# Kernel optimization log

Hardware: AMD Instinct MI355X
Metric: run time of the kernel (lower is better)

Reference implementation:

```python
import jax, jax.numpy as jnp
import numpy as np
from math import factorial

L_MAX = 8
N_POINTS = 1_000_000


def _make_F(l_max):
    n = (l_max + 1) * (l_max + 2) // 2
    F = np.empty((n,), dtype=np.float64)
    for l in range(l_max + 1):
        for m in range(l + 1):
            F[l * (l + 1) // 2 + m] = (-1) ** m * np.sqrt(
                (2 * l + 1) / (2 * np.pi) * factorial(l - m) / factorial(l + m)
            )
    return jnp.asarray(F, dtype=jnp.float32)


def setup_inputs() -> dict:
    key = jax.random.key(0)
    xyz = jax.random.normal(key, (N_POINTS, 3), dtype=jnp.float32)
    F = _make_F(L_MAX)
    return {"xyz": xyz, "F": F}


def reference(xyz, F):
    l_max = L_MAX
    # normalize to unit sphere
    rsq = jnp.sum(xyz ** 2, axis=1)
    u = xyz / jnp.sqrt(rsq)[:, None]
    x, y, z = u[:, 0], u[:, 1], u[:, 2]

    # associated-Legendre-like recurrence (same math/signs as the torch module)
    Q = {(0, 0): jnp.ones_like(x)}
    for l in range(1, l_max + 1):
        Q[(l, l)] = -(2 * l - 1) * Q[(l - 1, l - 1)]
        Q[(l, l - 1)] = -z * Q[(l, l)]
        for m in range(0, l - 1):
            Q[(l, m)] = ((2 * l - 1) * z * Q[(l - 1, m)] - (l + m - 1) * Q[(l - 2, m)]) / (l - m)

    # trig recurrence: s_m = Im[(x+iy)^m], c_m = Re[(x+iy)^m]
    s = [jnp.zeros_like(x)]
    c = [jnp.ones_like(x)]
    for m in range(1, l_max + 1):
        s.append(x * s[m - 1] + y * c[m - 1])
        c.append(x * c[m - 1] - y * s[m - 1])

    inv_sqrt2 = 1.0 / np.sqrt(2.0)
    cols = []  # ordered as Y[:, l*l + l + m]
    for l in range(l_max + 1):
        base = l * (l + 1) // 2
        for m in range(-l, 0):
            cols.append(F[base - m] * Q[(l, -m)] * s[-m])
        cols.append(F[base] * Q[(l, 0)] * inv_sqrt2)
        for m in range(1, l + 1):
            cols.append(F[base + m] * Q[(l, m)] * c[m])
    return jnp.stack(cols, axis=1)  # [N, (l_max+1)^2]
```

## Files before the change

### kernel.cpp

```cpp
#include <hip/hip_runtime.h>

constexpr int LMAX = 8;
constexpr int NCOL = (LMAX + 1) * (LMAX + 1);
constexpr int PTS  = 64;
constexpr int TILE_FLOATS = PTS * NCOL;
constexpr int VEC4_ITERS  = TILE_FLOATS / 4 / PTS;

__device__ __forceinline__ void emit_col(float* row, const float* __restrict__ F,
                                         int l, int m, float Q, float sm, float cm) {
    const int fbase = l * (l + 1) / 2;
    const int cbase = l * l + l;
    if (m == 0) {
        const float inv_sqrt2 = 0.70710678118654752440f;
        row[cbase] = F[fbase] * Q * inv_sqrt2;
    } else {
        float t = F[fbase + m] * Q;
        row[cbase - m] = t * sm;
        row[cbase + m] = t * cm;
    }
}

__global__ __launch_bounds__(PTS) void sh_kernel(const float* __restrict__ xyz,
                                                 const float* __restrict__ F,
                                                 float* __restrict__ out, int n) {
    __shared__ float tile[TILE_FLOATS];
    const int lane    = threadIdx.x;
    const int base_pt = blockIdx.x * PTS;
    const int i       = base_pt + lane;

    float x = 0.0f, y = 0.0f, z = 1.0f;
    if (i < n) {
        x = xyz[3 * i + 0];
        y = xyz[3 * i + 1];
        z = xyz[3 * i + 2];
    }
    const float rsq  = x * x + y * y + z * z;
    const float rinv = rsqrtf(rsq);
    x *= rinv; y *= rinv; z *= rinv;

    float* row = &tile[lane * NCOL];

    float Qmm = 1.0f;
    float sm = 0.0f, cm = 1.0f;

#pragma unroll
    for (int m = 0; m <= LMAX; ++m) {
        if (m > 0) {
            Qmm = -(float)(2 * m - 1) * Qmm;
            const float s_new = x * sm + y * cm;
            const float c_new = x * cm - y * sm;
            sm = s_new; cm = c_new;
        }
        float Qp = Qmm;
        emit_col(row, F, m, m, Qp, sm, cm);
        if (m < LMAX) {
            float Qc = (float)(2 * m + 1) * z * Qmm;
            emit_col(row, F, m + 1, m, Qc, sm, cm);
#pragma unroll
            for (int l = m + 2; l <= LMAX; ++l) {
                const float Qn = ((float)(2 * l - 1) * z * Qc
                                  - (float)(l + m - 1) * Qp) * (1.0f / (float)(l - m));
                Qp = Qc; Qc = Qn;
                emit_col(row, F, l, m, Qc, sm, cm);
            }
        }
    }

    __syncthreads();

    const long long tile_base = (long long)base_pt * NCOL;
    if (base_pt + PTS <= n) {
        const float4* src = (const float4*)tile;
        float4* dst = (float4*)(out + tile_base);
#pragma unroll
        for (int k = 0; k < VEC4_ITERS; ++k) {
            dst[k * PTS + lane] = src[k * PTS + lane];
        }
        out[tile_base + VEC4_ITERS * PTS * 4 + lane] = tile[VEC4_ITERS * PTS * 4 + lane];
    } else {
        const long long lim = (long long)n * NCOL;
        for (int k = lane; k < TILE_FLOATS; k += PTS) {
            const long long gi = tile_base + k;
            if (gi < lim) out[gi] = tile[k];
        }
    }
}

extern "C" void kernel_launch(void* const* d_in, const int* in_sizes, int n_in,
                              void* d_out, int out_size, void* d_ws, size_t ws_size,
                              hipStream_t stream) {
    const float* xyz = (const float*)d_in[0];
    const float* F   = (const float*)d_in[1];
    float* out       = (float*)d_out;
    const int n      = in_sizes[0] / 3;
    const int grid   = (n + PTS - 1) / PTS;
    sh_kernel<<<grid, PTS, 0, stream>>>(xyz, F, out, n);
}
```

Baseline: 335.8 us.

## Compute harmonics into registers and stage output through half-size LDS tile in two phases

The 81 outputs per point are now computed into a register array rather than written straight to shared memory. They are then staged into a tile half the previous size, 32 points at a time over two phases, with vectorized float4 writes into LDS. The smaller LDS footprint and the launch-bounds occupancy hint are meant to let more blocks reside per CU. The cost is higher register pressure from holding 81 floats per thread, extra barriers, and half the lanes idling during each staging phase.

Measured after the change: 359.5 us. +7.1%, slower.

```diff
diff --git a/kernel.cpp b/kernel.cpp
--- a/kernel.cpp
+++ b/kernel.cpp
@@ -3,27 +3,27 @@
 constexpr int LMAX = 8;
 constexpr int NCOL = (LMAX + 1) * (LMAX + 1);
 constexpr int PTS  = 64;
-constexpr int TILE_FLOATS = PTS * NCOL;
-constexpr int VEC4_ITERS  = TILE_FLOATS / 4 / PTS;
+constexpr int HALF = 32;
+constexpr int PHASE_FLOATS = HALF * NCOL;
 
-__device__ __forceinline__ void emit_col(float* row, const float* __restrict__ F,
+__device__ __forceinline__ void emit_col(float (&res)[NCOL], const float* __restrict__ F,
                                          int l, int m, float Q, float sm, float cm) {
     const int fbase = l * (l + 1) / 2;
     const int cbase = l * l + l;
     if (m == 0) {
         const float inv_sqrt2 = 0.70710678118654752440f;
-        row[cbase] = F[fbase] * Q * inv_sqrt2;
+        res[cbase] = F[fbase] * Q * inv_sqrt2;
     } else {
         float t = F[fbase + m] * Q;
-        row[cbase - m] = t * sm;
-        row[cbase + m] = t * cm;
+        res[cbase - m] = t * sm;
+        res[cbase + m] = t * cm;
     }
 }
 
-__global__ __launch_bounds__(PTS) void sh_kernel(const float* __restrict__ xyz,
-                                                 const float* __restrict__ F,
-                                                 float* __restrict__ out, int n) {
-    __shared__ float tile[TILE_FLOATS];
+__global__ __launch_bounds__(PTS, 4) void sh_kernel(const float* __restrict__ xyz,
+                                                    const float* __restrict__ F,
+                                                    float* __restrict__ out, int n) {
+    __shared__ float tile[PHASE_FLOATS];
     const int lane    = threadIdx.x;
     const int base_pt = blockIdx.x * PTS;
     const int i       = base_pt + lane;
@@ -38,7 +38,7 @@
     const float rinv = rsqrtf(rsq);
     x *= rinv; y *= rinv; z *= rinv;
 
-    float* row = &tile[lane * NCOL];
+    float res[NCOL];
 
     float Qmm = 1.0f;
     float sm = 0.0f, cm = 1.0f;
@@ -52,36 +52,52 @@
             sm = s_new; cm = c_new;
         }
         float Qp = Qmm;
-        emit_col(row, F, m, m, Qp, sm, cm);
+        emit_col(res, F, m, m, Qp, sm, cm);
         if (m < LMAX) {
             float Qc = (float)(2 * m + 1) * z * Qmm;
-            emit_col(row, F, m + 1, m, Qc, sm, cm);
+            emit_col(res, F, m + 1, m, Qc, sm, cm);
 #pragma unroll
             for (int l = m + 2; l <= LMAX; ++l) {
                 const float Qn = ((float)(2 * l - 1) * z * Qc
                                   - (float)(l + m - 1) * Qp) * (1.0f / (float)(l - m));
                 Qp = Qc; Qc = Qn;
-                emit_col(row, F, l, m, Qc, sm, cm);
+                emit_col(res, F, l, m, Qc, sm, cm);
             }
         }
     }
 
-    __syncthreads();
+    const long long lim = (long long)n * NCOL;
 
-    const long long tile_base = (long long)base_pt * NCOL;
-    if (base_pt + PTS <= n) {
-        const float4* src = (const float4*)tile;
-        float4* dst = (float4*)(out + tile_base);
 #pragma unroll
-        for (int k = 0; k < VEC4_ITERS; ++k) {
-            dst[k * PTS + lane] = src[k * PTS + lane];
+    for (int ph = 0; ph < 2; ++ph) {
+        __syncthreads();
+        const int sel = lane - ph * HALF;
+        if (sel >= 0 && sel < HALF) {
+            float* row = &tile[sel * NCOL];
+#pragma unroll
+            for (int k = 0; k < 20; ++k) {
+                float4 v = make_float4(res[4 * k + 0], res[4 * k + 1],
+                                       res[4 * k + 2], res[4 * k + 3]);
+                *(float4*)(row + 4 * k) = v;
+            }
+            row[80] = res[80];
         }
-        out[tile_base + VEC4_ITERS * PTS * 4 + lane] = tile[VEC4_ITERS * PTS * 4 + lane];
-    } else {
-        const long long lim = (long long)n * NCOL;
-        for (int k = lane; k < TILE_FLOATS; k += PTS) {
-            const long long gi = tile_base + k;
-            if (gi < lim) out[gi] = tile[k];
+        __syncthreads();
+
+        const long long off = (long long)base_pt * NCOL + (long long)ph * PHASE_FLOATS;
+        if (base_pt + PTS <= n) {
+            float4* dst       = (float4*)(out + off);
+            const float4* src = (const float4*)tile;
+#pragma unroll
+            for (int k = 0; k < 10; ++k) {
+                dst[k * PTS + lane] = src[k * PTS + lane];
+            }
+            if (lane < 8) dst[10 * PTS + lane] = src[10 * PTS + lane];
+        } else {
+            for (int k = lane; k < PHASE_FLOATS; k += PTS) {
+                const long long gi = off + k;
+                if (gi < lim) out[gi] = tile[k];
+            }
         }
     }
 }
```
